# Performance work log

Hardware: AMD Instinct MI355X
Metric: run time of the kernel (lower is better)

Reference implementation:

```python
import jax, jax.numpy as jnp
import numpy as np

B, C, L = 2, 256, 2048   # batch, emb_dim, seq_len
D, H = 64, 8             # d_model (per-head), n_heads
HD = D * H
EPS = 1e-8


def glob_ln(x, gamma, beta):
    # x: (B, C, L); normalize over all non-batch dims, affine over channel dim 1
    mean = jnp.mean(x, axis=(1, 2), keepdims=True)
    var = jnp.mean((x - mean) ** 2, axis=(1, 2), keepdims=True)
    normed = (x - mean) / jnp.sqrt(var + EPS)
    return gamma[None, :, None] * normed + beta[None, :, None]


def pos_encoding(length, dim):
    pos = jnp.arange(length, dtype=jnp.float32)[:, None]
    div = jnp.exp(jnp.arange(0, dim, 2, dtype=jnp.float32) * (-np.log(10000.0) / dim))
    ang = pos * div  # (L, dim/2)
    return jnp.stack([jnp.sin(ang), jnp.cos(ang)], axis=-1).reshape(length, dim)


def setup_inputs() -> dict:
    key = jax.random.key(0)
    ks = jax.random.split(key, 16)
    s_in = 1.0 / np.sqrt(C)
    s_hd = 1.0 / np.sqrt(HD)
    return {
        "x": jax.random.normal(ks[0], (B, C, L), dtype=jnp.float32),
        "Wq": jax.random.uniform(ks[1], (HD, C), minval=-s_in, maxval=s_in),
        "bq": jax.random.uniform(ks[2], (HD,), minval=-s_in, maxval=s_in),
        "Wk": jax.random.uniform(ks[3], (HD, C), minval=-s_in, maxval=s_in),
        "bk": jax.random.uniform(ks[4], (HD,), minval=-s_in, maxval=s_in),
        "Wv": jax.random.uniform(ks[5], (HD, C), minval=-s_in, maxval=s_in),
        "bv": jax.random.uniform(ks[6], (HD,), minval=-s_in, maxval=s_in),
        "Wo": jax.random.uniform(ks[7], (C, HD), minval=-s_hd, maxval=s_hd),
        "bo": jax.random.uniform(ks[8], (C,), minval=-s_hd, maxval=s_hd),
        "g_mha": jnp.ones((C,)), "b_mha": jnp.zeros((C,)),
        "conv_w": jax.random.uniform(ks[9], (C, C), minval=-s_in, maxval=s_in),
        "conv_b": jax.random.uniform(ks[10], (C,), minval=-s_in, maxval=s_in),
        "g_ffn": jnp.ones((C,)), "b_ffn": jnp.zeros((C,)),
        "alpha": jnp.float32(0.25),
        "g_out": jnp.ones((C,)), "b_out": jnp.zeros((C,)),
    }


def reference(x, Wq, bq, Wk, bk, Wv, bv, Wo, bo, g_mha, b_mha,
              conv_w, conv_b, g_ffn, b_ffn, alpha, g_out, b_out):
    scale = 1.0 / np.sqrt(D)
    t = jnp.transpose(x, (0, 2, 1))            # (B, L, C)
    t = t + pos_encoding(L, C)[None]
    # multi-head attention (self)
    q = (scale * (t @ Wq.T + bq)).reshape(B, L, H, D)
    k = (t @ Wk.T + bk).reshape(B, L, H, D)
    v = (t @ Wv.T + bv).reshape(B, L, H, D)
    scores = jnp.einsum('nlhd,nshd->nhls', q, k)  # (B, H, L, L)
    attn = jax.nn.softmax(scores, axis=-1)
    o = jnp.einsum('nhls,nshd->nlhd', attn, v).reshape(B, L, HD)
    t = t + (o @ Wo.T + bo)                    # residual
    y = glob_ln(jnp.transpose(t, (0, 2, 1)), g_mha, b_mha)  # (B, C, L)
    # FFN: 1x1 conv + GlobLN + PReLU
    f = jnp.einsum('bcl,oc->bol', y, conv_w) + conv_b[None, :, None]
    f = glob_ln(f, g_ffn, b_ffn)
    f = jnp.where(f >= 0, f, alpha * f)
    return glob_ln(f + y, g_out, b_out)
```

## Files before the change

kernel.cpp:

```cpp
#include <hip/hip_runtime.h>
#include <hip/hip_bf16.h>
#include <math.h>

#define BB   2
#define CC   256
#define LL   2048
#define DD   64
#define HH   8
#define HDIM 512
#define BLQ  (BB*LL)
#define EPSV 1e-8f
#define QSCALE (0.125f * 1.44269504088896f)

typedef __attribute__((ext_vector_type(8))) short short8;
typedef __attribute__((ext_vector_type(4))) float f32x4;

__device__ __forceinline__ float wred_sum(float v) {
#pragma unroll
    for (int off = 32; off > 0; off >>= 1) v += __shfl_down(v, off, 64);
    return v;
}
__device__ __forceinline__ unsigned pk(float a, float b) {
    unsigned r;
    asm("v_cvt_pk_bf16_f32 %0, %1, %2" : "=v"(r) : "v"(a), "v"(b));
    return r;
}
__device__ __forceinline__ float ex2(float x) {
    float r;
    asm("v_exp_f32 %0, %1" : "=v"(r) : "v"(x));
    return r;
}
__device__ __forceinline__ short8 ld_frag(const unsigned short* p) {
    union { short8 v; uint2 u[2]; } f;
    f.u[0] = *(const uint2*)p;
    f.u[1] = *(const uint2*)(p + 4);
    return f.v;
}

__global__ __launch_bounds__(256) void k_prep(const float* __restrict__ x,
                                              const float* __restrict__ Wq, const float* __restrict__ Wk,
                                              const float* __restrict__ Wv, const float* __restrict__ Wo,
                                              const float* __restrict__ Wc,
                                              float* __restrict__ t,
                                              unsigned short* __restrict__ tb,
                                              unsigned short* __restrict__ dqkv,
                                              unsigned short* __restrict__ dWo,
                                              unsigned short* __restrict__ dWc) {
    int bid = blockIdx.x;
    int tid = threadIdx.x;
    if (bid >= 256) {
        int idx = ((bid - 256) * 256 + tid) * 4;
        const float* s; unsigned short* d;
        if (idx < 131072)      { s = Wq + idx;          d = dqkv + idx; }
        else if (idx < 262144) { s = Wk + idx - 131072; d = dqkv + idx; }
        else if (idx < 393216) { s = Wv + idx - 262144; d = dqkv + idx; }
        else if (idx < 524288) { s = Wo + idx - 393216; d = dWo + idx - 393216; }
        else                   { s = Wc + idx - 524288; d = dWc + idx - 524288; }
        float4 v = *(const float4*)s;
        uint2 u; u.x = pk(v.x, v.y); u.y = pk(v.z, v.w);
        *(uint2*)d = u;
        return;
    }
    __shared__ float tr[64][65];
    int l0 = (bid & 31) * 64, c0 = ((bid >> 5) & 3) * 64, b = bid >> 7;
    int r = tid >> 2, q = tid & 3;
#pragma unroll
    for (int p = 0; p < 4; ++p) {
        int lc = 4 * (q + 4 * p);
        float4 v = *(const float4*)&x[((size_t)(b * CC + c0 + r)) * LL + l0 + lc];
        tr[lc + 0][r] = v.x; tr[lc + 1][r] = v.y; tr[lc + 2][r] = v.z; tr[lc + 3][r] = v.w;
    }
    __syncthreads();
    int lg = l0 + r;
#pragma unroll
    for (int p = 0; p < 4; ++p) {
        int cc = 4 * (q + 4 * p);
        float4 v = *(const float4*)&tr[r][cc];
        float pe[4];
#pragma unroll
        for (int i = 0; i < 4; ++i) {
            int cg = c0 + cc + i;
            float freq = __expf((float)(cg & ~1) * (-9.210340371976184f / (float)CC));
            float ang = (float)lg * freq;
            pe[i] = (cg & 1) ? __cosf(ang) : __sinf(ang);
        }
        v.x += pe[0]; v.y += pe[1]; v.z += pe[2]; v.w += pe[3];
        size_t o = ((size_t)(b * LL + lg)) * CC + c0 + cc;
        *(float4*)&t[o] = v;
        uint2 u; u.x = pk(v.x, v.y); u.y = pk(v.z, v.w);
        *(uint2*)&tb[o] = u;
    }
}

#define MLDK 68
__global__ __launch_bounds__(256) void k_mm(const unsigned short* __restrict__ A,
                                            const unsigned short* __restrict__ W,
                                            const float* __restrict__ b0,
                                            const float* __restrict__ b1,
                                            const float* __restrict__ b2,
                                            const float* resid,
                                            float* out, unsigned short* outb,
                                            float* pstat,
                                            int mode, int M, int N, int K) {
    __shared__ unsigned short As[2][64][MLDK];
    __shared__ unsigned short Ws[2][64][MLDK];
    __shared__ float rs[4][2];
    int tid = threadIdx.x;
    int w = tid >> 6, lane = tid & 63, g = lane >> 4, qi = lane & 15;
    int bm = blockIdx.x * 64, bn = blockIdx.y * 64;
    int wr = w >> 1, wc = w & 1;
    int srow = tid >> 2, sq = tid & 3;
    bool vseg = (mode == 1) && (bn >= 1024);
    f32x4 acc[2][2];
    acc[0][0] = acc[0][1] = acc[1][0] = acc[1][1] = (f32x4){0.f, 0.f, 0.f, 0.f};
    uint4 ra[2], rw[2];
#pragma unroll
    for (int p = 0; p < 2; ++p) {
        ra[p] = *(const uint4*)&A[(size_t)(bm + srow) * K + (sq + 4 * p) * 8];
        rw[p] = *(const uint4*)&W[(size_t)(bn + srow) * K + (sq + 4 * p) * 8];
    }
    int nt = K >> 6;
    for (int it = 0; it < nt; ++it) {
        int buf = it & 1;
#pragma unroll
        for (int p = 0; p < 2; ++p) {
            *(uint2*)&As[buf][srow][(sq + 4 * p) * 8]     = make_uint2(ra[p].x, ra[p].y);
            *(uint2*)&As[buf][srow][(sq + 4 * p) * 8 + 4] = make_uint2(ra[p].z, ra[p].w);
            *(uint2*)&Ws[buf][srow][(sq + 4 * p) * 8]     = make_uint2(rw[p].x, rw[p].y);
            *(uint2*)&Ws[buf][srow][(sq + 4 * p) * 8 + 4] = make_uint2(rw[p].z, rw[p].w);
        }
        __syncthreads();
        if (it + 1 < nt) {
            int k0 = (it + 1) << 6;
#pragma unroll
            for (int p = 0; p < 2; ++p) {
                ra[p] = *(const uint4*)&A[(size_t)(bm + srow) * K + k0 + (sq + 4 * p) * 8];
                rw[p] = *(const uint4*)&W[(size_t)(bn + srow) * K + k0 + (sq + 4 * p) * 8];
            }
        }
#pragma unroll
        for (int c = 0; c < 2; ++c) {
            short8 wf0 = ld_frag(&Ws[buf][wr * 32 + 0  + qi][c * 32 + 8 * g]);
            short8 wf1 = ld_frag(&Ws[buf][wr * 32 + 16 + qi][c * 32 + 8 * g]);
            short8 af0 = ld_frag(&As[buf][wc * 32 + 0  + qi][c * 32 + 8 * g]);
            short8 af1 = ld_frag(&As[buf][wc * 32 + 16 + qi][c * 32 + 8 * g]);
            if (!vseg) {
                acc[0][0] = __builtin_amdgcn_mfma_f32_16x16x32_bf16(wf0, af0, acc[0][0], 0, 0, 0);
                acc[0][1] = __builtin_amdgcn_mfma_f32_16x16x32_bf16(wf0, af1, acc[0][1], 0, 0, 0);
                acc[1][0] = __builtin_amdgcn_mfma_f32_16x16x32_bf16(wf1, af0, acc[1][0], 0, 0, 0);
                acc[1][1] = __builtin_amdgcn_mfma_f32_16x16x32_bf16(wf1, af1, acc[1][1], 0, 0, 0);
            } else {
                acc[0][0] = __builtin_amdgcn_mfma_f32_16x16x32_bf16(af0, wf0, acc[0][0], 0, 0, 0);
                acc[0][1] = __builtin_amdgcn_mfma_f32_16x16x32_bf16(af0, wf1, acc[0][1], 0, 0, 0);
                acc[1][0] = __builtin_amdgcn_mfma_f32_16x16x32_bf16(af1, wf0, acc[1][0], 0, 0, 0);
                acc[1][1] = __builtin_amdgcn_mfma_f32_16x16x32_bf16(af1, wf1, acc[1][1], 0, 0, 0);
            }
        }
    }
    if (mode == 0) {
        float s = 0.f, s2 = 0.f;
#pragma unroll
        for (int fi = 0; fi < 2; ++fi)
#pragma unroll
            for (int fj = 0; fj < 2; ++fj) {
                int n0 = bn + wr * 32 + fi * 16 + 4 * g;
                int m  = bm + wc * 32 + fj * 16 + qi;
                float4 bi = *(const float4*)&b0[n0];
                float4 v;
                v.x = acc[fi][fj][0] + bi.x; v.y = acc[fi][fj][1] + bi.y;
                v.z = acc[fi][fj][2] + bi.z; v.w = acc[fi][fj][3] + bi.w;
                if (resid) {
                    float4 rv = *(const float4*)&resid[(size_t)m * N + n0];
                    v.x += rv.x; v.y += rv.y; v.z += rv.z; v.w += rv.w;
                }
                *(float4*)&out[(size_t)m * N + n0] = v;
                s  += (v.x + v.y) + (v.z + v.w);
                s2 += v.x * v.x + v.y * v.y + v.z * v.z + v.w * v.w;
            }
        if (pstat) {
            s = wred_sum(s); s2 = wred_sum(s2);
            if (lane == 0) { rs[w][0] = s; rs[w][1] = s2; }
            __syncthreads();
            if (tid == 0) {
                int bid = blockIdx.y * gridDim.x + blockIdx.x;
                pstat[bid * 2 + 0] = rs[0][0] + rs[1][0] + rs[2][0] + rs[3][0];
                pstat[bid * 2 + 1] = rs[0][1] + rs[1][1] + rs[2][1] + rs[3][1];
            }
        }
    } else if (!vseg) {
        int seg = bn >> 9;
        const float* bs = seg ? b1 : b0;
        float sc = seg ? 1.f : QSCALE;
#pragma unroll
        for (int fi = 0; fi < 2; ++fi)
#pragma unroll
            for (int fj = 0; fj < 2; ++fj) {
                int nn0 = (bn & 511) + wr * 32 + fi * 16 + 4 * g;
                int m   = bm + wc * 32 + fj * 16 + qi;
                int b = m >> 11, l = m & (LL - 1);
                int h = nn0 >> 6, d0 = nn0 & 63;
                float4 bi = *(const float4*)&bs[nn0];
                uint2 u;
                u.x = pk(sc * (acc[fi][fj][0] + bi.x), sc * (acc[fi][fj][1] + bi.y));
                u.y = pk(sc * (acc[fi][fj][2] + bi.z), sc * (acc[fi][fj][3] + bi.w));
                *(uint2*)&outb[(size_t)seg * 2097152 +
                               (((size_t)(b * HH + h)) * LL + l) * DD + d0] = u;
            }
    } else {
#pragma unroll
        for (int fi = 0; fi < 2; ++fi)
#pragma unroll
            for (int fj = 0; fj < 2; ++fj) {
                int m0 = bm + wc * 32 + fi * 16 + 4 * g;
                int nn = (bn & 511) + wr * 32 + fj * 16 + qi;
                int b = m0 >> 11, l0 = m0 & (LL - 1);
                int h = nn >> 6, d = nn & 63;
                float bi = b2[nn];
                uint2 u;
                u.x = pk(acc[fi][fj][0] + bi, acc[fi][fj][1] + bi);
                u.y = pk(acc[fi][fj][2] + bi, acc[fi][fj][3] + bi);
                *(uint2*)&outb[(size_t)2 * 2097152 +
                               (((size_t)(b * HH + h)) * DD + d) * LL + l0] = u;
            }
    }
}

#define LDK 68
__global__ __launch_bounds__(256) void k_attn(const unsigned short* __restrict__ QKV,
                                              unsigned short* __restrict__ o) {
    int bh = blockIdx.x;
    int h = bh & 7, b = bh >> 3;
    int tid = threadIdx.x;
    int w = tid >> 6, lane = tid & 63, g = lane >> 4, qi = lane & 15;
    int q0 = blockIdx.y * 64 + w * 16;
    __shared__ unsigned short Ks[2][64][LDK];
    __shared__ unsigned short Vts[2][64][LDK];
    __shared__ unsigned short Pw[4][16][LDK];
    const unsigned short* Qg = QKV + (size_t)bh * LL * DD;
    const unsigned short* Kg = QKV + 2097152 + (size_t)bh * LL * DD;
    const unsigned short* Vg = QKV + (size_t)2 * 2097152 + (size_t)bh * DD * LL;

    short8 qf[2];
#pragma unroll
    for (int c = 0; c < 2; ++c)
        qf[c] = *(const short8*)&Qg[(size_t)(q0 + qi) * DD + c * 32 + 8 * g];

    f32x4 ot[4];
#pragma unroll
    for (int db = 0; db < 4; ++db) ot[db] = (f32x4){0.f, 0.f, 0.f, 0.f};
    float m = -INFINITY, sum = 0.f;

    int srow = tid >> 2, sq = tid & 3;
    uint4 kr[2], vr[2];
#pragma unroll
    for (int p = 0; p < 2; ++p) {
        kr[p] = *(const uint4*)&Kg[(size_t)srow * DD + (sq + 4 * p) * 8];
        vr[p] = *(const uint4*)&Vg[(size_t)srow * LL + (sq + 4 * p) * 8];
    }
    for (int it = 0; it < LL / 64; ++it) {
        int buf = it & 1;
#pragma unroll
        for (int p = 0; p < 2; ++p) {
            *(uint2*)&Ks[buf][srow][(sq + 4 * p) * 8]      = make_uint2(kr[p].x, kr[p].y);
            *(uint2*)&Ks[buf][srow][(sq + 4 * p) * 8 + 4]  = make_uint2(kr[p].z, kr[p].w);
            *(uint2*)&Vts[buf][srow][(sq + 4 * p) * 8]     = make_uint2(vr[p].x, vr[p].y);
            *(uint2*)&Vts[buf][srow][(sq + 4 * p) * 8 + 4] = make_uint2(vr[p].z, vr[p].w);
        }
        __syncthreads();
        if (it + 1 < LL / 64) {
            int s1 = (it + 1) * 64;
#pragma unroll
            for (int p = 0; p < 2; ++p) {
                kr[p] = *(const uint4*)&Kg[(size_t)(s1 + srow) * DD + (sq + 4 * p) * 8];
                vr[p] = *(const uint4*)&Vg[(size_t)srow * LL + s1 + (sq + 4 * p) * 8];
            }
        }
        f32x4 st[4];
        __builtin_amdgcn_s_setprio(1);
#pragma unroll
        for (int sb = 0; sb < 4; ++sb) {
            f32x4 a = (f32x4){0.f, 0.f, 0.f, 0.f};
#pragma unroll
            for (int c = 0; c < 2; ++c) {
                short8 kf = ld_frag(&Ks[buf][sb * 16 + qi][c * 32 + 8 * g]);
                a = __builtin_amdgcn_mfma_f32_16x16x32_bf16(kf, qf[c], a, 0, 0, 0);
            }
            st[sb] = a;
        }
        __builtin_amdgcn_s_setprio(0);
        float t0 = fmaxf(fmaxf(st[0][0], st[0][1]), fmaxf(st[0][2], st[0][3]));
        float t1 = fmaxf(fmaxf(st[1][0], st[1][1]), fmaxf(st[1][2], st[1][3]));
        float t2 = fmaxf(fmaxf(st[2][0], st[2][1]), fmaxf(st[2][2], st[2][3]));
        float t3 = fmaxf(fmaxf(st[3][0], st[3][1]), fmaxf(st[3][2], st[3][3]));
        float tmax = fmaxf(fmaxf(t0, t1), fmaxf(t2, t3));
        tmax = fmaxf(tmax, __shfl_xor(tmax, 16, 64));
        tmax = fmaxf(tmax, __shfl_xor(tmax, 32, 64));
        if (!__all(tmax - m <= 8.f)) {
            float mnew = fmaxf(m, tmax);
            float corr = ex2(m - mnew);
            m = mnew;
            sum *= corr;
#pragma unroll
            for (int db = 0; db < 4; ++db)
#pragma unroll
                for (int r = 0; r < 4; ++r) ot[db][r] *= corr;
        }
        float ps = 0.f;
#pragma unroll
        for (int sb = 0; sb < 4; ++sb) {
            float p0 = ex2(st[sb][0] - m);
            float p1 = ex2(st[sb][1] - m);
            float p2 = ex2(st[sb][2] - m);
            float p3 = ex2(st[sb][3] - m);
            ps += (p0 + p1) + (p2 + p3);
            uint2 w2; w2.x = pk(p0, p1); w2.y = pk(p2, p3);
            *(uint2*)&Pw[w][qi][sb * 16 + 4 * g] = w2;
        }
        sum += ps;
        __builtin_amdgcn_s_setprio(1);
#pragma unroll
        for (int db = 0; db < 4; ++db)
#pragma unroll
            for (int sc = 0; sc < 2; ++sc) {
                short8 vf = ld_frag(&Vts[buf][db * 16 + qi][sc * 32 + 8 * g]);
                short8 pf = ld_frag(&Pw[w][qi][sc * 32 + 8 * g]);
                ot[db] = __builtin_amdgcn_mfma_f32_16x16x32_bf16(vf, pf, ot[db], 0, 0, 0);
            }
        __builtin_amdgcn_s_setprio(0);
    }
    sum += __shfl_xor(sum, 16, 64);
    sum += __shfl_xor(sum, 32, 64);
    float rinv = 1.f / sum;
#pragma unroll
    for (int db = 0; db < 4; ++db) {
        int d0 = db * 16 + 4 * g;
        uint2 u;
        u.x = pk(ot[db][0] * rinv, ot[db][1] * rinv);
        u.y = pk(ot[db][2] * rinv, ot[db][3] * rinv);
        *(uint2*)&o[((size_t)(b * LL + q0 + qi)) * HDIM + h * DD + d0] = u;
    }
}

__global__ __launch_bounds__(256) void k_ln(const float* in,
                                            const float* __restrict__ g,
                                            const float* __restrict__ be,
                                            const float* __restrict__ pin,
                                            const float* __restrict__ add,
                                            const float* __restrict__ alpha_ptr,
                                            float* out, unsigned short* outb,
                                            float* pout) {
    __shared__ float rs[4][2];
    int tid = threadIdx.x;
    int b = blockIdx.x >> 9;
    float s = 0.f, s2 = 0.f;
    if (tid < 128) {
        int pidx = (tid >> 5) * 64 + b * 32 + (tid & 31);
        s  = pin[pidx * 2 + 0];
        s2 = pin[pidx * 2 + 1];
    }
    s = wred_sum(s); s2 = wred_sum(s2);
    if ((tid & 63) == 0 && tid < 128) { rs[tid >> 6][0] = s; rs[tid >> 6][1] = s2; }
    __syncthreads();
    float S = rs[0][0] + rs[1][0], S2 = rs[0][1] + rs[1][1];
    float mean = S / (float)(CC * LL);
    float inv  = rsqrtf(S2 / (float)(CC * LL) - mean * mean + EPSV);

    int idx = (blockIdx.x * 256 + tid) * 4;
    int c = idx & (CC - 1);
    float4 v  = *(const float4*)&in[idx];
    float4 gg = *(const float4*)&g[c];
    float4 bb = *(const float4*)&be[c];
    v.x = (v.x - mean) * inv * gg.x + bb.x;
    v.y = (v.y - mean) * inv * gg.y + bb.y;
    v.z = (v.z - mean) * inv * gg.z + bb.z;
    v.w = (v.w - mean) * inv * gg.w + bb.w;
    if (alpha_ptr) {
        float al = alpha_ptr[0];
        v.x = v.x >= 0.f ? v.x : al * v.x;
        v.y = v.y >= 0.f ? v.y : al * v.y;
        v.z = v.z >= 0.f ? v.z : al * v.z;
        v.w = v.w >= 0.f ? v.w : al * v.w;
    }
    if (add) {
        float4 a = *(const float4*)&add[idx];
        v.x += a.x; v.y += a.y; v.z += a.z; v.w += a.w;
    }
    *(float4*)&out[idx] = v;
    if (outb) {
        uint2 u; u.x = pk(v.x, v.y); u.y = pk(v.z, v.w);
        *(uint2*)&outb[idx] = u;
    }
    if (pout) {
        float os  = (v.x + v.y) + (v.z + v.w);
        float os2 = v.x * v.x + v.y * v.y + v.z * v.z + v.w * v.w;
        os = wred_sum(os); os2 = wred_sum(os2);
        __syncthreads();
        if ((tid & 63) == 0) { rs[tid >> 6][0] = os; rs[tid >> 6][1] = os2; }
        __syncthreads();
        if (tid == 0) {
            pout[blockIdx.x * 2 + 0] = rs[0][0] + rs[1][0] + rs[2][0] + rs[3][0];
            pout[blockIdx.x * 2 + 1] = rs[0][1] + rs[1][1] + rs[2][1] + rs[3][1];
        }
    }
}

__global__ __launch_bounds__(256) void k_ln_t(const float* __restrict__ in,
                                              const float* __restrict__ g,
                                              const float* __restrict__ be,
                                              const float* __restrict__ pin,
                                              float* __restrict__ out) {
    __shared__ float tr[64][65];
    __shared__ float rs[4][2];
    int l0 = blockIdx.x * 64, c0 = blockIdx.y * 64, b = blockIdx.z;
    int tid = threadIdx.x, r = tid >> 2, q = tid & 3;
    float s  = pin[(b * 512 + tid) * 2 + 0] + pin[(b * 512 + 256 + tid) * 2 + 0];
    float s2 = pin[(b * 512 + tid) * 2 + 1] + pin[(b * 512 + 256 + tid) * 2 + 1];
    s = wred_sum(s); s2 = wred_sum(s2);
    if ((tid & 63) == 0) { rs[tid >> 6][0] = s; rs[tid >> 6][1] = s2; }
    __syncthreads();
    float S = rs[0][0] + rs[1][0] + rs[2][0] + rs[3][0];
    float S2 = rs[0][1] + rs[1][1] + rs[2][1] + rs[3][1];
    float mean = S / (float)(CC * LL);
    float inv  = rsqrtf(S2 / (float)(CC * LL) - mean * mean + EPSV);
#pragma unroll
    for (int p = 0; p < 4; ++p) {
        int cc = 4 * (q + 4 * p);
        float4 v  = *(const float4*)&in[((size_t)(b * LL + l0 + r)) * CC + c0 + cc];
        float4 gg = *(const float4*)&g[c0 + cc];
        float4 bb = *(const float4*)&be[c0 + cc];
        tr[cc + 0][r] = (v.x - mean) * inv * gg.x + bb.x;
        tr[cc + 1][r] = (v.y - mean) * inv * gg.y + bb.y;
        tr[cc + 2][r] = (v.z - mean) * inv * gg.z + bb.z;
        tr[cc + 3][r] = (v.w - mean) * inv * gg.w + bb.w;
    }
    __syncthreads();
#pragma unroll
    for (int p = 0; p < 4; ++p) {
        int ll = 4 * (q + 4 * p);
        float4 v = *(const float4*)&tr[r][ll];
        *(float4*)&out[((size_t)(b * CC + c0 + r)) * LL + l0 + ll] = v;
    }
}

extern "C" void kernel_launch(void* const* d_in, const int* in_sizes, int n_in,
                              void* d_out, int out_size, void* d_ws, size_t ws_size,
                              hipStream_t stream) {
    const float* x      = (const float*)d_in[0];
    const float* Wq     = (const float*)d_in[1];
    const float* bq     = (const float*)d_in[2];
    const float* Wk     = (const float*)d_in[3];
    const float* bk     = (const float*)d_in[4];
    const float* Wv     = (const float*)d_in[5];
    const float* bv     = (const float*)d_in[6];
    const float* Wo     = (const float*)d_in[7];
    const float* bo     = (const float*)d_in[8];
    const float* g_mha  = (const float*)d_in[9];
    const float* b_mha  = (const float*)d_in[10];
    const float* conv_w = (const float*)d_in[11];
    const float* conv_b = (const float*)d_in[12];
    const float* g_ffn  = (const float*)d_in[13];
    const float* b_ffn  = (const float*)d_in[14];
    const float* alpha  = (const float*)d_in[15];
    const float* g_out  = (const float*)d_in[16];
    const float* b_out  = (const float*)d_in[17];
    float* out = (float*)d_out;

    float* ws = (float*)d_ws;
    float* t             = ws;
    unsigned short* tb   = (unsigned short*)(ws + 1048576);
    unsigned short* QKVb = (unsigned short*)(ws + 1572864);
    float* f             = ws + 1572864;
    unsigned short* ybf  = (unsigned short*)(ws + 2621440);
    unsigned short* obuf = (unsigned short*)(ws + 4718592);
    unsigned short* Wqkvb= (unsigned short*)(ws + 5767168);
    unsigned short* Wob  = (unsigned short*)(ws + 5963776);
    unsigned short* Wcb  = (unsigned short*)(ws + 6029312);
    float* pstatA        = ws + 6062080;
    float* pstatB        = ws + 6062592;
    float* pstatC        = ws + 6063104;

    k_prep<<<832, 256, 0, stream>>>(x, Wq, Wk, Wv, Wo, conv_w, t, tb, Wqkvb, Wob, Wcb);

    dim3 gqkv(BLQ / 64, 1536 / 64);
    k_mm<<<gqkv, 256, 0, stream>>>(tb, Wqkvb, bq, bk, bv, nullptr, nullptr, QKVb,
                                   nullptr, 1, BLQ, 1536, CC);

    dim3 gattn(HH * BB, LL / 64);
    k_attn<<<gattn, 256, 0, stream>>>(QKVb, obuf);

    dim3 go(BLQ / 64, CC / 64);
    k_mm<<<go, 256, 0, stream>>>(obuf, Wob, bo, nullptr, nullptr, t, t, nullptr,
                                 pstatA, 0, BLQ, CC, HDIM);

    k_ln<<<1024, 256, 0, stream>>>(t, g_mha, b_mha, pstatA, nullptr, nullptr,
                                   t, ybf, nullptr);

    k_mm<<<go, 256, 0, stream>>>(ybf, Wcb, conv_b, nullptr, nullptr, nullptr, f, nullptr,
                                 pstatB, 0, BLQ, CC, CC);

    k_ln<<<1024, 256, 0, stream>>>(f, g_ffn, b_ffn, pstatB, t, alpha,
                                   f, nullptr, pstatC);

    k_ln_t<<<dim3(LL / 64, CC / 64, BB), 256, 0, stream>>>(f, g_out, b_out, pstatC, out);
}
```

Baseline: 92.94 us.

## Split attention over key dimension into two halves with log-sum-exp merge

The attention kernel now splits the key/value sequence into two halves along a third grid dimension. Each half writes a normalized partial output plus a log-sum-exp value, and a new merge kernel combines the two partials with softmax weights. This doubles the number of blocks (from 512 to 1024), which should improve occupancy across the many CUs. The cost is an extra kernel launch, extra global traffic for the partial outputs, and bf16 rounding of the partial results before merging.

New measurement: 94.64 us. About the same (+1.8%).

```diff
diff --git a/kernel.cpp b/kernel.cpp
--- a/kernel.cpp
+++ b/kernel.cpp
@@ -29,6 +29,14 @@
     float r;
     asm("v_exp_f32 %0, %1" : "=v"(r) : "v"(x));
     return r;
+}
+__device__ __forceinline__ float lg2(float x) {
+    float r;
+    asm("v_log_f32 %0, %1" : "=v"(r) : "v"(x));
+    return r;
+}
+__device__ __forceinline__ float bf2f(unsigned short v) {
+    union { unsigned u; float f; } c; c.u = ((unsigned)v) << 16; return c.f;
 }
 __device__ __forceinline__ short8 ld_frag(const unsigned short* p) {
     union { short8 v; uint2 u[2]; } f;
@@ -227,9 +235,13 @@
 
 #define LDK 68
 __global__ __launch_bounds__(256) void k_attn(const unsigned short* __restrict__ QKV,
-                                              unsigned short* __restrict__ o) {
+                                              unsigned short* __restrict__ op0,
+                                              unsigned short* __restrict__ op1,
+                                              float* __restrict__ ls) {
     int bh = blockIdx.x;
     int h = bh & 7, b = bh >> 3;
+    int z = blockIdx.z;
+    int sb0 = z << 10;
     int tid = threadIdx.x;
     int w = tid >> 6, lane = tid & 63, g = lane >> 4, qi = lane & 15;
     int q0 = blockIdx.y * 64 + w * 16;
@@ -254,10 +266,10 @@
     uint4 kr[2], vr[2];
 #pragma unroll
     for (int p = 0; p < 2; ++p) {
-        kr[p] = *(const uint4*)&Kg[(size_t)srow * DD + (sq + 4 * p) * 8];
-        vr[p] = *(const uint4*)&Vg[(size_t)srow * LL + (sq + 4 * p) * 8];
-    }
-    for (int it = 0; it < LL / 64; ++it) {
+        kr[p] = *(const uint4*)&Kg[(size_t)(sb0 + srow) * DD + (sq + 4 * p) * 8];
+        vr[p] = *(const uint4*)&Vg[(size_t)srow * LL + sb0 + (sq + 4 * p) * 8];
+    }
+    for (int it = 0; it < 16; ++it) {
         int buf = it & 1;
 #pragma unroll
         for (int p = 0; p < 2; ++p) {
@@ -267,8 +279,8 @@
             *(uint2*)&Vts[buf][srow][(sq + 4 * p) * 8 + 4] = make_uint2(vr[p].z, vr[p].w);
         }
         __syncthreads();
-        if (it + 1 < LL / 64) {
-            int s1 = (it + 1) * 64;
+        if (it + 1 < 16) {
+            int s1 = sb0 + (it + 1) * 64;
 #pragma unroll
             for (int p = 0; p < 2; ++p) {
                 kr[p] = *(const uint4*)&Kg[(size_t)(s1 + srow) * DD + (sq + 4 * p) * 8];
@@ -331,14 +343,48 @@
     sum += __shfl_xor(sum, 16, 64);
     sum += __shfl_xor(sum, 32, 64);
     float rinv = 1.f / sum;
+    unsigned short* op = z ? op1 : op0;
 #pragma unroll
     for (int db = 0; db < 4; ++db) {
         int d0 = db * 16 + 4 * g;
         uint2 u;
         u.x = pk(ot[db][0] * rinv, ot[db][1] * rinv);
         u.y = pk(ot[db][2] * rinv, ot[db][3] * rinv);
-        *(uint2*)&o[((size_t)(b * LL + q0 + qi)) * HDIM + h * DD + d0] = u;
-    }
+        *(uint2*)&op[((size_t)(b * LL + q0 + qi)) * HDIM + h * DD + d0] = u;
+    }
+    if (g == 0) ls[(z << 15) + bh * LL + q0 + qi] = m + lg2(sum);
+}
+
+__global__ __launch_bounds__(256) void k_amerge(const unsigned short* op0,
+                                                const unsigned short* op1,
+                                                const float* __restrict__ ls,
+                                                unsigned short* out) {
+    int flat = (blockIdx.x * 256 + threadIdx.x) * 8;
+    int tt = flat >> 9;
+    int h  = (flat >> 6) & 7;
+    int b  = tt >> 11, l = tt & (LL - 1);
+    int bh = b * HH + h;
+    float l0 = ls[bh * LL + l];
+    float l1 = ls[(1 << 15) + bh * LL + l];
+    float M  = fmaxf(l0, l1);
+    float w0 = ex2(l0 - M), w1 = ex2(l1 - M);
+    float inv = 1.f / (w0 + w1);
+    w0 *= inv; w1 *= inv;
+    uint4 a = *(const uint4*)&op0[flat];
+    uint4 c = *(const uint4*)&op1[flat];
+    const unsigned* au = (const unsigned*)&a;
+    const unsigned* cu = (const unsigned*)&c;
+    uint4 r;
+    unsigned* ru = (unsigned*)&r;
+#pragma unroll
+    for (int i = 0; i < 4; ++i) {
+        float a0 = bf2f((unsigned short)(au[i] & 0xffff));
+        float a1 = bf2f((unsigned short)(au[i] >> 16));
+        float c0 = bf2f((unsigned short)(cu[i] & 0xffff));
+        float c1 = bf2f((unsigned short)(cu[i] >> 16));
+        ru[i] = pk(w0 * a0 + w1 * c0, w0 * a1 + w1 * c1);
+    }
+    *(uint4*)&out[flat] = r;
 }
 
 __global__ __launch_bounds__(256) void k_ln(const float* in,
@@ -478,6 +524,8 @@
     float* pstatA        = ws + 6062080;
     float* pstatB        = ws + 6062592;
     float* pstatC        = ws + 6063104;
+    unsigned short* op1  = (unsigned short*)(ws + 6065152);
+    float* lsbuf         = ws + 7113728;
 
     k_prep<<<832, 256, 0, stream>>>(x, Wq, Wk, Wv, Wo, conv_w, t, tb, Wqkvb, Wob, Wcb);
 
@@ -485,8 +533,9 @@
     k_mm<<<gqkv, 256, 0, stream>>>(tb, Wqkvb, bq, bk, bv, nullptr, nullptr, QKVb,
                                    nullptr, 1, BLQ, 1536, CC);
 
-    dim3 gattn(HH * BB, LL / 64);
-    k_attn<<<gattn, 256, 0, stream>>>(QKVb, obuf);
+    dim3 gattn(HH * BB, LL / 64, 2);
+    k_attn<<<gattn, 256, 0, stream>>>(QKVb, obuf, op1, lsbuf);
+    k_amerge<<<1024, 256, 0, stream>>>(obuf, op1, lsbuf, obuf);
 
     dim3 go(BLQ / 64, CC / 64);
     k_mm<<<go, 256, 0, stream>>>(obuf, Wob, bo, nullptr, nullptr, t, t, nullptr,
```
